# Optimization experiments

Hardware: AMD Instinct MI355X
Metric: run time of the kernel (lower is better)

Reference implementation:

```python
import math
import jax, jax.numpy as jnp
import numpy as np

BS = 4; C = 128; D = 128; NH = 4; NL = 2; NP = 8
SHAPES = [(64, 96), (32, 48)]            # (H, W) per level
STARTS = [0, SHAPES[0][0] * SHAPES[0][1]]  # level_start_index


def lrelu(x):
    return jnp.where(x >= 0, x, 0.1 * x)


def conv2d(x, w, b):
    y = jax.lax.conv_general_dilated(x, w, (1, 1), [(1, 1), (1, 1)],
                                     dimension_numbers=('NCHW', 'OIHW', 'NCHW'))
    return y + b[None, :, None, None]


def pos_enc_sine(bs, H, W, npf=64, T=10000.0):
    # DETR PositionEmbeddingSine (normalize=True), mask of ones -> cumsum = index+1
    scale = 2.0 * math.pi
    eps = 1e-6
    y = (jnp.arange(1, H + 1, dtype=jnp.float32) / (H + eps) * scale)[:, None]
    x = (jnp.arange(1, W + 1, dtype=jnp.float32) / (W + eps) * scale)[None, :]
    y = jnp.broadcast_to(y, (H, W))
    x = jnp.broadcast_to(x, (H, W))
    dim_t = T ** (2.0 * (jnp.arange(npf) // 2).astype(jnp.float32) / npf)
    px = x[..., None] / dim_t
    py = y[..., None] / dim_t
    def interleave(p):
        return jnp.stack([jnp.sin(p[..., 0::2]), jnp.cos(p[..., 1::2])], -1).reshape(H, W, npf)
    pos = jnp.concatenate([interleave(py), interleave(px)], -1)  # [H,W,2*npf]
    return jnp.broadcast_to(pos.transpose(2, 0, 1)[None], (bs, 2 * npf, H, W))


def ref_points(bs, H, W):
    ys = (jnp.arange(H, dtype=jnp.float32) + 0.5) / H
    xs = (jnp.arange(W, dtype=jnp.float32) + 0.5) / W
    gy, gx = jnp.meshgrid(ys, xs, indexing='ij')
    ref = jnp.stack([gx.reshape(-1), gy.reshape(-1)], -1)  # [hw, 2] (x, y)
    return jnp.broadcast_to(ref[None, :, None, :], (bs, H * W, 1, 2))


def sample_level(v, loc, Hl, Wl):
    # v: [bs, Hl*Wl, nh, d]; loc: [bs, nq, nh, np, 2] in [0,1] -> grid_sample bilinear, zero pad
    bs, nq, nh, npts, _ = loc.shape
    d = v.shape[-1]
    x = loc[..., 0] * Wl - 0.5
    y = loc[..., 1] * Hl - 0.5
    x0f = jnp.floor(x); y0f = jnp.floor(y)
    fx = x - x0f; fy = y - y0f
    x0 = x0f.astype(jnp.int32); y0 = y0f.astype(jnp.int32)
    def gather(xi, yi):
        valid = (xi >= 0) & (xi < Wl) & (yi >= 0) & (yi < Hl)
        idx = jnp.clip(yi, 0, Hl - 1) * Wl + jnp.clip(xi, 0, Wl - 1)  # [bs,nq,nh,np]
        idx = idx.transpose(0, 1, 3, 2).reshape(bs, nq * npts, nh)
        g = jnp.take_along_axis(v, idx[..., None], axis=1)  # [bs,nq*np,nh,d]
        g = g.reshape(bs, nq, npts, nh, d).transpose(0, 1, 3, 2, 4)  # [bs,nq,nh,np,d]
        return g * valid[..., None]
    w00 = (1 - fx) * (1 - fy); w01 = fx * (1 - fy); w10 = (1 - fx) * fy; w11 = fx * fy
    return (gather(x0, y0) * w00[..., None] + gather(x0 + 1, y0) * w01[..., None]
            + gather(x0, y0 + 1) * w10[..., None] + gather(x0 + 1, y0 + 1) * w11[..., None])


def msda(value, loc, weights):
    # value [bs,Nv,nh,d], loc [bs,nq,nh,nl,np,2], weights [bs,nq,nh,nl,np]
    out = 0.0
    for l, (Hl, Wl) in enumerate(SHAPES):
        v_l = value[:, STARTS[l]:STARTS[l] + Hl * Wl]
        s = sample_level(v_l, loc[:, :, :, l], Hl, Wl)  # [bs,nq,nh,np,d]
        out = out + jnp.einsum('bqhpd,bqhp->bqhd', s, weights[:, :, :, l])
    bs, nq, nh, d = out.shape
    return out.reshape(bs, nq, nh * d)


def block(query, value, qloc, so_w, so_b, aw_w, aw_b, op_w, op_b):
    bs, nq, _ = query.shape
    off = (query @ so_w + so_b).reshape(bs, nq, NH, NL, NP, 2)
    aw = jax.nn.softmax((query @ aw_w + aw_b).reshape(bs, nq, NH, NL * NP), -1)
    aw = aw.reshape(bs, nq, NH, NL, NP)
    norm = jnp.array([[w, h] for (h, w) in SHAPES], jnp.float32)  # [nl,2] = (W,H)
    loc = qloc[:, :, None, :, None, :] + off / norm[None, None, None, :, None, :]
    return msda(value, loc, aw) @ op_w + op_b  # dropout = identity (eval)


def _forward(feat0_l0, feat0_l1, feat1_l0, feat1_l1,
             cw1, cb1, cw2, cb2, cw3, cb3, vw, vb, lvl_emb,
             so_w0, so_b0, aw_w0, aw_b0, op_w0, op_b0,
             so_w1, so_b1, aw_w1, aw_b1, op_w1, op_b1):
    bs = feat0_l0.shape[0]
    H1, W1 = SHAPES[-1]
    # scale_conv stem on feature0_list[-1]
    q = lrelu(conv2d(feat0_l1, cw1, cb1))
    q = lrelu(conv2d(q, cw2, cb2))
    q = lrelu(conv2d(q, cw3, cb3))
    q = q + pos_enc_sine(bs, H1, W1, npf=D // 2)
    qloc = ref_points(bs, H1, W1)  # [bs, hw, 1, 2]
    # flatten levels + level embeds
    f0 = jnp.concatenate([f.reshape(bs, C, -1) + lvl_emb[l][None, :, None]
                          for l, f in enumerate([feat0_l0, feat0_l1])], axis=2)
    f1 = jnp.concatenate([f.reshape(bs, C, -1) + lvl_emb[l][None, :, None]
                          for l, f in enumerate([feat1_l0, feat1_l1])], axis=2)
    cat = jnp.concatenate([f0, f1], axis=1)  # [bs, 2C, Nv]
    value = jnp.einsum('oc,bcn->bno', vw, cat) + vb  # 1x1 Conv1d -> [bs, Nv, D]
    value = jnp.broadcast_to(value[:, :, None, :], (bs, value.shape[1], NH, D))
    query = q.reshape(bs, D, -1).transpose(0, 2, 1)  # [bs, hw, D]
    query = block(query, value, qloc, so_w0, so_b0, aw_w0, aw_b0, op_w0, op_b0)
    query = block(query, value, qloc, so_w1, so_b1, aw_w1, aw_b1, op_w1, op_b1)
    return query.reshape(bs, H1, W1, D).transpose(0, 3, 1, 2)


def setup_inputs() -> dict:
    key = jax.random.key(0)
    ks = iter(jax.random.split(key, 32))
    def rn(shape, s=1.0):
        return jax.random.normal(next(ks), shape, jnp.float32) * s
    inp = {}
    inp['feat0_l0'] = rn((BS, C, SHAPES[0][0], SHAPES[0][1]))
    inp['feat0_l1'] = rn((BS, C, SHAPES[1][0], SHAPES[1][1]))
    inp['feat1_l0'] = rn((BS, C, SHAPES[0][0], SHAPES[0][1]))
    inp['feat1_l1'] = rn((BS, C, SHAPES[1][0], SHAPES[1][1]))
    inp['cw1'] = rn((2 * D, C, 3, 3), 0.03); inp['cb1'] = rn((2 * D,), 0.01)
    inp['cw2'] = rn((D, 2 * D, 3, 3), 0.03); inp['cb2'] = rn((D,), 0.01)
    inp['cw3'] = rn((D, D, 3, 3), 0.03); inp['cb3'] = rn((D,), 0.01)
    inp['vw'] = rn((D, 2 * C), 0.05); inp['vb'] = rn((D,), 0.01)
    inp['lvl_emb'] = rn((NL, C), 0.05)
    for i in range(2):
        inp[f'so_w{i}'] = rn((D, NH * NL * NP * 2), 0.02)
        inp[f'so_b{i}'] = rn((NH * NL * NP * 2,), 0.5)
        inp[f'aw_w{i}'] = rn((D, NH * NL * NP), 0.02)
        inp[f'aw_b{i}'] = rn((NH * NL * NP,), 0.01)
        inp[f'op_w{i}'] = rn((NH * D, D), 0.05)
        inp[f'op_b{i}'] = rn((D,), 0.01)
    return inp


def reference(feat0_l0, feat0_l1, feat1_l0, feat1_l1,
              cw1, cb1, cw2, cb2, cw3, cb3, vw, vb, lvl_emb,
              so_w0, so_b0, aw_w0, aw_b0, op_w0, op_b0,
              so_w1, so_b1, aw_w1, aw_b1, op_w1, op_b1):
    return _forward(feat0_l0, feat0_l1, feat1_l0, feat1_l1,
                    cw1, cb1, cw2, cb2, cw3, cb3, vw, vb, lvl_emb,
                    so_w0, so_b0, aw_w0, aw_b0, op_w0, op_b0,
                    so_w1, so_b1, aw_w1, aw_b1, op_w1, op_b1)
```

## Files before the change

### kernel.cpp

```cpp
#include <hip/hip_runtime.h>
#include <hip/hip_bf16.h>

typedef unsigned short u16;
typedef u16   u16x8 __attribute__((ext_vector_type(8)));
typedef short s16x8 __attribute__((ext_vector_type(8)));
typedef float f32x4 __attribute__((ext_vector_type(4)));

__device__ __forceinline__ float bf2f(u16 u) {
    union { unsigned int i; float f; } v; v.i = ((unsigned int)u) << 16; return v.f;
}
__device__ __forceinline__ u16 f2bf(float f) {
    unsigned int x = __float_as_uint(f);
    return (u16)((x + 0x7fffu + ((x >> 16) & 1u)) >> 16);
}
__device__ __forceinline__ float ldv(const void* p, size_t i, int f32) {
    return f32 ? ((const float*)p)[i] : bf2f(((const u16*)p)[i]);
}

template<int ACT, int OUTM, int OUT_BF16, int BN>
__device__ __forceinline__ void gemm_body(
    u16* __restrict__ smem, int bid,
    const u16* __restrict__ A, const u16* __restrict__ Bt,
    const u16* __restrict__ bias, void* __restrict__ Cv,
    int M, int K, int ldc, int nbase, const int* __restrict__ flag)
{
    constexpr int NF = BN >> 4;
    u16 (*As)[72] = (u16(*)[72])smem;
    u16 (*Bs)[72] = (u16(*)[72])(smem + 4608);

    const int t    = threadIdx.x;
    const int wv   = t >> 6, lane = t & 63;
    const int fr   = lane & 15, fg = lane >> 4;
    const int tiles_m = M >> 6;
    const int bm = bid % tiles_m, bn = bid / tiles_m;
    const int m0 = bm << 6, n0 = bn * BN;

    f32x4 acc[NF] = {};
    const int srow = t >> 2;
    const int scol = (t & 3) << 4;
    const int brow = (BN == 64) ? srow : (t >> 3);
    const int bcol = (BN == 64) ? scol : ((t & 7) << 3);
    const u16* Ap = A  + (size_t)(m0 + srow) * K + scol;
    const u16* Bp = Bt + (size_t)(n0 + brow) * K + bcol;

    const int ns = K >> 6;
    uint4 av0 = *(const uint4*)Ap, av1 = *(const uint4*)(Ap + 8);
    uint4 bv0 = *(const uint4*)Bp, bv1 = {0,0,0,0};
    if constexpr (BN == 64) bv1 = *(const uint4*)(Bp + 8);
    for (int s = 0; s < ns; ++s) {
        __syncthreads();
        *(uint4*)&As[srow][scol]     = av0;  *(uint4*)&As[srow][scol + 8] = av1;
        *(uint4*)&Bs[brow][bcol]     = bv0;
        if constexpr (BN == 64) *(uint4*)&Bs[brow][bcol + 8] = bv1;
        __syncthreads();
        if (s + 1 < ns) {
            const u16* An = Ap + ((s + 1) << 6);
            const u16* Bn = Bp + ((s + 1) << 6);
            av0 = *(const uint4*)An;  av1 = *(const uint4*)(An + 8);
            bv0 = *(const uint4*)Bn;
            if constexpr (BN == 64) bv1 = *(const uint4*)(Bn + 8);
        }
        union U { uint4 q; s16x8 v; };
        #pragma unroll
        for (int kk = 0; kk < 2; ++kk) {
            U af; af.q = *(const uint4*)&As[(wv << 4) + fr][(kk << 5) + (fg << 3)];
            U bf[NF];
            #pragma unroll
            for (int j = 0; j < NF; ++j)
                bf[j].q = *(const uint4*)&Bs[(j << 4) + fr][(kk << 5) + (fg << 3)];
            #pragma unroll
            for (int j = 0; j < NF; ++j)
                acc[j] = __builtin_amdgcn_mfma_f32_16x16x32_bf16(af.v, bf[j].v, acc[j], 0, 0, 0);
        }
    }

    float vv[NF][4];
    #pragma unroll
    for (int r = 0; r < 4; ++r) {
        float bvv = bf2f(bias[m0 + (wv << 4) + (fg << 2) + r]);
        #pragma unroll
        for (int j = 0; j < NF; ++j) {
            float v = acc[j][r] + bvv;
            if (ACT) v = (v >= 0.f) ? v : 0.1f * v;
            vv[j][r] = v;
        }
    }

    if constexpr (OUTM == 0) {
        #pragma unroll
        for (int j = 0; j < NF; ++j)
            #pragma unroll
            for (int r = 0; r < 4; ++r) {
                size_t idx = (size_t)(m0 + (wv << 4) + (fg << 2) + r) * ldc
                           + (nbase + n0 + (j << 4) + fr);
                if (OUT_BF16) ((u16*)Cv)[idx] = f2bf(vv[j][r]);
                else          ((float*)Cv)[idx] = vv[j][r];
            }
    } else if constexpr (OUTM == 1) {
        __syncthreads();
        u16* bb = smem;
        #pragma unroll
        for (int j = 0; j < NF; ++j)
            #pragma unroll
            for (int r = 0; r < 4; ++r)
                bb[((j << 4) + fr) * 72 + (wv << 4) + (fg << 2) + r] = f2bf(vv[j][r]);
        __syncthreads();
        if constexpr (BN == 64) {
            int row = t >> 2, seg = (t & 3) << 4;
            const uint4* src = (const uint4*)&bb[row * 72 + seg];
            uint4* dst = (uint4*)((u16*)Cv + (size_t)(nbase + n0 + row) * M + m0 + seg);
            dst[0] = src[0];
            dst[1] = src[1];
        } else {
            int row = t >> 3, seg = (t & 7) << 3;
            const uint4* src = (const uint4*)&bb[row * 72 + seg];
            uint4* dst = (uint4*)((u16*)Cv + (size_t)(nbase + n0 + row) * M + m0 + seg);
            dst[0] = src[0];
        }
    } else {
        __syncthreads();
        constexpr int LDB = BN + 8;
        u16* bb = smem;
        #pragma unroll
        for (int j = 0; j < NF; ++j)
            #pragma unroll
            for (int r = 0; r < 4; ++r)
                bb[((wv << 4) + (fg << 2) + r) * LDB + (j << 4) + fr] = f2bf(vv[j][r]);
        __syncthreads();
        int f32o = *flag;
        constexpr int EPT = BN / 4;
        int mrow = t >> 2, seg = (t & 3) * EPT;
        int b = n0 / 1536, hw0 = (n0 % 1536) + seg;
        size_t base = (size_t)(b * 128 + m0 + mrow) * 1536 + hw0;
        if (!f32o) {
            #pragma unroll
            for (int q = 0; q < EPT / 8; ++q)
                *(uint4*)((u16*)Cv + base + q * 8) = *(const uint4*)&bb[mrow * LDB + seg + q * 8];
        } else {
            float* dst = (float*)Cv + base;
            #pragma unroll
            for (int j = 0; j < EPT; ++j) dst[j] = bf2f(bb[mrow * LDB + seg + j]);
        }
    }
}

template<int CIN, int POS, int BN>
__device__ __forceinline__ void conv_body(
    u16* __restrict__ smem, int bid,
    const u16* __restrict__ A, const u16* __restrict__ X,
    const u16* __restrict__ bias, u16* __restrict__ Cv, int M)
{
    constexpr int NF = BN >> 4;
    u16 (*As)[72] = (u16(*)[72])smem;
    u16 (*Bs)[72] = (u16(*)[72])(smem + 4608);

    constexpr int NK2 = CIN / 64;
    constexpr int TOT = 9 * NK2;

    const int t    = threadIdx.x;
    const int wv   = t >> 6, lane = t & 63;
    const int fr   = lane & 15, fg = lane >> 4;
    const int tiles_m = M >> 6;
    const int bm = bid % tiles_m, bn = bid / tiles_m;
    const int m0 = bm << 6, n0 = bn * BN;

    const int srow = t >> 2;
    const int scol = (t & 3) << 4;
    const int brow = (BN == 64) ? srow : (t >> 3);
    const int bcol = (BN == 64) ? scol : ((t & 7) << 3);
    const int n  = n0 + brow;
    const int hw = n % 1536;
    const int hp = hw / 48, wp = hw % 48;
    const u16* Ar = A + (size_t)(m0 + srow) * (9 * CIN) + scol;

    f32x4 acc[NF] = {};

    auto ld = [&](int s, uint4& a0, uint4& a1, uint4& b0, uint4& b1) {
        int tap = s / NK2, k0 = (s % NK2) << 6;
        int dy = tap / 3 - 1, dx = tap % 3 - 1;
        bool vr = ((unsigned)(hp + dy) < 32u) && ((unsigned)(wp + dx) < 48u);
        const u16* Ap = Ar + tap * CIN + k0;
        a0 = *(const uint4*)Ap;  a1 = *(const uint4*)(Ap + 8);
        if (vr) {
            const u16* Bp = X + (size_t)(n + dy * 48 + dx) * CIN + bcol + k0;
            b0 = *(const uint4*)Bp;
            if constexpr (BN == 64) b1 = *(const uint4*)(Bp + 8);
        } else {
            b0 = uint4{0,0,0,0};  b1 = uint4{0,0,0,0};
        }
    };

    uint4 av0, av1, bv0, bv1;
    ld(0, av0, av1, bv0, bv1);
    for (int s = 0; s < TOT; ++s) {
        __syncthreads();
        *(uint4*)&As[srow][scol]     = av0;  *(uint4*)&As[srow][scol + 8] = av1;
        *(uint4*)&Bs[brow][bcol]     = bv0;
        if constexpr (BN == 64) *(uint4*)&Bs[brow][bcol + 8] = bv1;
        __syncthreads();
        if (s + 1 < TOT) ld(s + 1, av0, av1, bv0, bv1);
        union U { uint4 q; s16x8 v; };
        #pragma unroll
        for (int kk = 0; kk < 2; ++kk) {
            U af; af.q = *(const uint4*)&As[(wv << 4) + fr][(kk << 5) + (fg << 3)];
            U bf[NF];
            #pragma unroll
            for (int j = 0; j < NF; ++j)
                bf[j].q = *(const uint4*)&Bs[(j << 4) + fr][(kk << 5) + (fg << 3)];
            #pragma unroll
            for (int j = 0; j < NF; ++j)
                acc[j] = __builtin_amdgcn_mfma_f32_16x16x32_bf16(af.v, bf[j].v, acc[j], 0, 0, 0);
        }
    }

    float vv[NF][4];
    #pragma unroll
    for (int r = 0; r < 4; ++r) {
        float bvv = bf2f(bias[m0 + (wv << 4) + (fg << 2) + r]);
        #pragma unroll
        for (int j = 0; j < NF; ++j) {
            float v = acc[j][r] + bvv;
            vv[j][r] = (v >= 0.f) ? v : 0.1f * v;
        }
    }

    if (POS) {
        const float TWO_PI = 6.283185307179586f;
        #pragma unroll
        for (int j = 0; j < NF; ++j) {
            int ntok = n0 + (j << 4) + fr;
            int hw2 = ntok % 1536;
            int hp2 = hw2 / 48, wp2 = hw2 % 48;
            float yv = (float)(hp2 + 1) * (TWO_PI / (32.f + 1e-6f));
            float xv = (float)(wp2 + 1) * (TWO_PI / (48.f + 1e-6f));
            #pragma unroll
            for (int r = 0; r < 4; ++r) {
                int d = m0 + (wv << 4) + (fg << 2) + r;
                int mm = (d & 63) >> 1;
                float dim = exp2f((float)mm * (13.287712379549449f / 32.f));
                float val = ((d < 64) ? yv : xv) / dim;
                vv[j][r] += (d & 1) ? cosf(val) : sinf(val);
            }
        }
    }

    __syncthreads();
    u16* bb = smem;
    #pragma unroll
    for (int j = 0; j < NF; ++j)
        #pragma unroll
        for (int r = 0; r < 4; ++r)
            bb[((j << 4) + fr) * 72 + (wv << 4) + (fg << 2) + r] = f2bf(vv[j][r]);
    __syncthreads();
    if constexpr (BN == 64) {
        int row = t >> 2, seg = (t & 3) << 4;
        const uint4* src = (const uint4*)&bb[row * 72 + seg];
        uint4* dst = (uint4*)(Cv + (size_t)(n0 + row) * M + m0 + seg);
        dst[0] = src[0];
        dst[1] = src[1];
    } else {
        int row = t >> 3, seg = (t & 7) << 3;
        const uint4* src = (const uint4*)&bb[row * 72 + seg];
        uint4* dst = (uint4*)(Cv + (size_t)(n0 + row) * M + m0 + seg);
        dst[0] = src[0];
    }
}

template<int CIN, int POS, int BN>
__global__ __launch_bounds__(256) void conv_gemm(
    const u16* __restrict__ A, const u16* __restrict__ X,
    const u16* __restrict__ bias, u16* __restrict__ Cv, int M)
{
    __shared__ __align__(16) u16 smem[9216];
    conv_body<CIN, POS, BN>(smem, blockIdx.x, A, X, bias, Cv, M);
}

__global__ __launch_bounds__(256) void val_conv1_k(
    const u16* __restrict__ AVW, const u16* __restrict__ CATT,
    const u16* __restrict__ vb, u16* __restrict__ VAL,
    const u16* __restrict__ AW1, const u16* __restrict__ X0,
    const u16* __restrict__ cb1, u16* __restrict__ CH1)
{
    __shared__ __align__(16) u16 smem[9216];
    int bid = blockIdx.x;
    if (bid < 960) gemm_body<0, 1, 1, 64>(smem, bid, AVW, CATT, vb, VAL, 128, 256, 0, 0, nullptr);
    else           conv_body<128, 0, 64>(smem, bid - 960, AW1, X0, cb1, CH1, 256);
}

template<int OUTM>
__global__ __launch_bounds__(256) void attn_fused(
    const u16* __restrict__ QT, const u16* __restrict__ APJ,
    const u16* __restrict__ BPJ, const u16* __restrict__ VAL,
    const u16* __restrict__ AOP, const u16* __restrict__ OB,
    void* __restrict__ OUT, const int* __restrict__ flag)
{
    __shared__ __align__(16) char lds[46144];
    u16*   qs  = (u16*)lds;
    u16*   Ss  = (u16*)(lds + 4352);
    float* PAs = (float*)(lds + 20992);
    float* XYs = (float*)(lds + 33856);
    float* LGs = (float*)(lds + 42048);

    const int t  = threadIdx.x;
    const int wv = t >> 6, lane = t & 63;
    const int fr = lane & 15, fg = lane >> 4;
    const int bid = blockIdx.x;
    const int tok0 = ((bid & 7) * 48 + (bid >> 3)) << 4;

    union U { uint4 q; s16x8 v; };

    {
        int tok = t >> 4, seg = (t & 15) << 3;
        *(uint4*)&qs[tok * 136 + seg] = *(const uint4*)&QT[(size_t)(tok0 + tok) * 128 + seg];
    }
    __syncthreads();

    {
        f32x4 pacc[3] = {};
        #pragma unroll
        for (int ks = 0; ks < 4; ++ks) {
            U bf; bf.q = *(const uint4*)&qs[fr * 136 + ks * 32 + (fg << 3)];
            #pragma unroll
            for (int j = 0; j < 3; ++j) {
                int m = ((wv * 3 + j) << 4) + fr;
                U af; af.q = *(const uint4*)&APJ[(size_t)m * 128 + ks * 32 + (fg << 3)];
                pacc[j] = __builtin_amdgcn_mfma_f32_16x16x32_bf16(af.v, bf.v, pacc[j], 0, 0, 0);
            }
        }
        #pragma unroll
        for (int j = 0; j < 3; ++j) {
            int mb = (wv * 3 + j) << 4;
            #pragma unroll
            for (int r = 0; r < 4; ++r) {
                int m = mb + (fg << 2) + r;
                PAs[fr * 201 + m] = pacc[j][r] + bf2f(BPJ[m]);
            }
        }
    }
    __syncthreads();

    #pragma unroll
    for (int i = 0; i < 4; ++i) {
        int slot = t + i * 256;
        int tok = slot >> 6, s = slot & 63;
        int h = s >> 4, l = (s >> 3) & 1, p = s & 7;
        int orow = h * 32 + l * 16 + p * 2;
        int lrow = 128 + h * 16 + l * 8 + p;
        float offx = PAs[tok * 201 + orow];
        float offy = PAs[tok * 201 + orow + 1];
        int gtok = tok0 + tok;
        int hw = gtok % 1536;
        int hp = hw / 48, wp = hw % 48;
        float Wl = l ? 48.f : 96.f, Hl = l ? 32.f : 64.f;
        float locx = (wp + 0.5f) / 48.f + offx / Wl;
        float locy = (hp + 0.5f) / 32.f + offy / Hl;
        XYs[(tok * 64 + s) * 2]     = locx * Wl - 0.5f;
        XYs[(tok * 64 + s) * 2 + 1] = locy * Hl - 0.5f;
        LGs[tok * 64 + s] = PAs[tok * 201 + lrow];
    }
    __syncthreads();

    float awr[4];
    #pragma unroll
    for (int i = 0; i < 4; ++i) {
        int slot = t + i * 256;
        int tok = slot >> 6, s = slot & 63;
        const float* G = &LGs[tok * 64 + (s & ~15)];
        float mx = -1e30f;
        for (int j2 = 0; j2 < 16; ++j2) mx = fmaxf(mx, G[j2]);
        float sum = 0.f;
        for (int j2 = 0; j2 < 16; ++j2) sum += expf(G[j2] - mx);
        awr[i] = expf(LGs[tok * 64 + s] - mx) / sum;
    }
    __syncthreads();
    #pragma unroll
    for (int i = 0; i < 4; ++i) {
        int slot = t + i * 256;
        LGs[(slot >> 6) * 64 + (slot & 63)] = awr[i];
    }
    __syncthreads();

    {
        const int tokg = t >> 5, sub = t & 31, h = sub >> 3, seg = sub & 7;
        #pragma unroll
        for (int round = 0; round < 2; ++round) {
            int tok = round * 8 + tokg;
            int b = (tok0 + tok) / 1536;
            float acc[16];
            #pragma unroll
            for (int j = 0; j < 16; ++j) acc[j] = 0.f;
            #pragma unroll 2
            for (int s16i = 0; s16i < 16; ++s16i) {
                int s = h * 16 + s16i;
                int l = (s16i >> 3) & 1;
                int iWl = l ? 48 : 96, iHl = l ? 32 : 64;
                int vrow = b * 7680 + (l ? 6144 : 0);
                float x  = XYs[(tok * 64 + s) * 2];
                float y  = XYs[(tok * 64 + s) * 2 + 1];
                float aw = LGs[tok * 64 + s];
                float xf = floorf(x), yf = floorf(y);
                float fx = x - xf, fy = y - yf;
                int ix = (int)xf, iy = (int)yf;
                bool vx0 = (unsigned)ix < (unsigned)iWl, vx1 = (unsigned)(ix + 1) < (unsigned)iWl;
                bool vy0 = (unsigned)iy < (unsigned)iHl, vy1 = (unsigned)(iy + 1) < (unsigned)iHl;
                float w0 = (vx0 && vy0) ? (1.f - fx) * (1.f - fy) * aw : 0.f;
                float w1 = (vx1 && vy0) ? fx * (1.f - fy) * aw : 0.f;
                float w2 = (vx0 && vy1) ? (1.f - fx) * fy * aw : 0.f;
                float w3 = (vx1 && vy1) ? fx * fy * aw : 0.f;
                int i0 = (vx0 && vy0) ? vrow + iy * iWl + ix           : 0;
                int i1 = (vx1 && vy0) ? vrow + iy * iWl + ix + 1       : 0;
                int i2 = (vx0 && vy1) ? vrow + (iy + 1) * iWl + ix     : 0;
                int i3 = (vx1 && vy1) ? vrow + (iy + 1) * iWl + ix + 1 : 0;
                const u16* p0 = VAL + (size_t)i0 * 128 + (seg << 4);
                const u16* p1 = VAL + (size_t)i1 * 128 + (seg << 4);
                const u16* p2 = VAL + (size_t)i2 * 128 + (seg << 4);
                const u16* p3 = VAL + (size_t)i3 * 128 + (seg << 4);
                u16x8 v0a = *(const u16x8*)p0, v0b = *(const u16x8*)(p0 + 8);
                u16x8 v1a = *(const u16x8*)p1, v1b = *(const u16x8*)(p1 + 8);
                u16x8 v2a = *(const u16x8*)p2, v2b = *(const u16x8*)(p2 + 8);
                u16x8 v3a = *(const u16x8*)p3, v3b = *(const u16x8*)(p3 + 8);
                #pragma unroll
                for (int j = 0; j < 8; ++j) {
                    acc[j]     += w0 * bf2f(v0a[j]) + w1 * bf2f(v1a[j])
                                + w2 * bf2f(v2a[j]) + w3 * bf2f(v3a[j]);
                    acc[8 + j] += w0 * bf2f(v0b[j]) + w1 * bf2f(v1b[j])
                                + w2 * bf2f(v2b[j]) + w3 * bf2f(v3b[j]);
                }
            }
            u16x8 o0, o1;
            #pragma unroll
            for (int j = 0; j < 8; ++j) { o0[j] = f2bf(acc[j]); o1[j] = f2bf(acc[8 + j]); }
            u16* sp = &Ss[tok * 520 + (h << 7) + (seg << 4)];
            *(u16x8*)sp = o0;
            *(u16x8*)(sp + 8) = o1;
        }
    }
    __syncthreads();

    {
        f32x4 oacc[2] = {};
        for (int ks = 0; ks < 16; ++ks) {
            U bf; bf.q = *(const uint4*)&Ss[fr * 520 + ks * 32 + (fg << 3)];
            #pragma unroll
            for (int j = 0; j < 2; ++j) {
                int m = ((wv * 2 + j) << 4) + fr;
                U af; af.q = *(const uint4*)&AOP[(size_t)m * 512 + ks * 32 + (fg << 3)];
                oacc[j] = __builtin_amdgcn_mfma_f32_16x16x32_bf16(af.v, bf.v, oacc[j], 0, 0, 0);
            }
        }
        #pragma unroll
        for (int j = 0; j < 2; ++j) {
            int mb = (wv * 2 + j) << 4;
            #pragma unroll
            for (int r = 0; r < 4; ++r) {
                int m = mb + (fg << 2) + r;
                qs[fr * 136 + m] = f2bf(oacc[j][r] + bf2f(OB[m]));
            }
        }
    }
    __syncthreads();

    if constexpr (OUTM == 0) {
        int tok = t >> 4, m0 = (t & 15) << 3;
        *(uint4*)((u16*)OUT + (size_t)(tok0 + tok) * 128 + m0) = *(const uint4*)&qs[tok * 136 + m0];
    } else {
        int f32o = *flag;
        int m = t & 127, grp = t >> 7;
        int b = tok0 / 1536, hw0 = (tok0 % 1536) + (grp << 3);
        size_t base = (size_t)(b * 128 + m) * 1536 + hw0;
        if (!f32o) {
            u16x8 o;
            #pragma unroll
            for (int j = 0; j < 8; ++j) o[j] = qs[((grp << 3) + j) * 136 + m];
            *(u16x8*)((u16*)OUT + base) = o;
        } else {
            #pragma unroll
            for (int j = 0; j < 8; ++j)
                ((float*)OUT)[base + j] = bf2f(qs[((grp << 3) + j) * 136 + m]);
        }
    }
}

struct P21 { const void* p[21]; };

__global__ __launch_bounds__(256) void prep_fused(
    P21 a, const void* __restrict__ f00, const void* __restrict__ f01,
    const void* __restrict__ f10, const void* __restrict__ f11,
    int* __restrict__ FLAG,
    u16* AW1, u16* AW2, u16* AW3, u16* AVW,
    u16* APJ0, u16* APJ1, u16* AOP0, u16* AOP1,
    u16* BPJ0, u16* BPJ1, u16* SB,
    u16* CATT, u16* X0)
{
    __shared__ __align__(16) u16 Ts[128 * 66];
    const int t = threadIdx.x;
    unsigned int w = ((const unsigned int*)f00)[t];
    float pa = fabsf(bf2f((u16)(w & 0xFFFFu)));
    int cnt = __syncthreads_count(pa > 1e-6f && pa < 1e4f);
    const int f32 = (cnt < 128);
    const int bid = blockIdx.x;
    if (bid == 0 && t == 0) *FLAG = f32;

    if (bid < 3718) {
        int g = bid * 256 + t;
        if (g < 294912) { int m = g / 1152, rem = g % 1152, tap = rem >> 7, ci = rem & 127;
            AW1[g] = f2bf(ldv(a.p[0], (size_t)m * 1152 + ci * 9 + tap, f32)); return; }
        g -= 294912;
        if (g < 294912) { int m = g / 2304, rem = g % 2304, tap = rem >> 8, ci = rem & 255;
            AW2[g] = f2bf(ldv(a.p[2], (size_t)m * 2304 + ci * 9 + tap, f32)); return; }
        g -= 294912;
        if (g < 147456) { int m = g / 1152, rem = g % 1152, tap = rem >> 7, ci = rem & 127;
            AW3[g] = f2bf(ldv(a.p[4], (size_t)m * 1152 + ci * 9 + tap, f32)); return; }
        g -= 147456;
        if (g < 32768) { AVW[g] = f2bf(ldv(a.p[6], g, f32)); return; }
        g -= 32768;
        if (g < 24576) { int o = g >> 7, d = g & 127;
            APJ0[g] = f2bf(o < 128 ? ldv(a.p[9], d * 128 + o, f32)
                                   : ldv(a.p[11], d * 64 + (o - 128), f32)); return; }
        g -= 24576;
        if (g < 24576) { int o = g >> 7, d = g & 127;
            APJ1[g] = f2bf(o < 128 ? ldv(a.p[15], d * 128 + o, f32)
                                   : ldv(a.p[17], d * 64 + (o - 128), f32)); return; }
        g -= 24576;
        if (g < 65536) { int o = g >> 9, k = g & 511; AOP0[g] = f2bf(ldv(a.p[13], k * 128 + o, f32)); return; }
        g -= 65536;
        if (g < 65536) { int o = g >> 9, k = g & 511; AOP1[g] = f2bf(ldv(a.p[19], k * 128 + o, f32)); return; }
        g -= 65536;
        if (g < 192) { BPJ0[g] = f2bf(g < 128 ? ldv(a.p[10], g, f32) : ldv(a.p[12], g - 128, f32)); return; }
        g -= 192;
        if (g < 192) { BPJ1[g] = f2bf(g < 128 ? ldv(a.p[16], g, f32) : ldv(a.p[18], g - 128, f32)); return; }
        g -= 192;
        if (g < 1152) {
            const int off[8] = {0, 256, 384, 512, 640, 896, 1024, 1152};
            const int src[7] = {1, 3, 5, 7, 8, 14, 20};
            int s = 0;
            #pragma unroll
            for (int i = 1; i < 7; ++i) s += (g >= off[i]);
            SB[g] = f2bf(ldv(a.p[src[s]], g - off[s], f32));
        }
        return;
    }

    const void* src; u16* dst;
    int b, hw0, HW, rowlen, coloff, lvl, addemb;
    if (bid < 4678) {
        int g = bid - 3718;
        int half = g & 1;  g >>= 1;
        b = g / 120;  int tile = g % 120;
        lvl = (tile >= 96) ? 1 : 0;
        int tl = lvl ? tile - 96 : tile;
        hw0 = tl << 6;
        HW = lvl ? 1536 : 6144;
        src = (half == 0) ? (lvl ? f01 : f00) : (lvl ? f11 : f10);
        dst = CATT + (size_t)(b * 7680 + lvl * 6144 + hw0) * 256;
        rowlen = 256; coloff = half << 7; addemb = 1;
    } else {
        int g = bid - 4678;
        b = g / 24;  hw0 = (g % 24) << 6;
        HW = 1536; src = f01;
        dst = X0 + (size_t)(b * 1536 + hw0) * 128;
        rowlen = 128; coloff = 0; lvl = 1; addemb = 0;
    }

    {
        int c = t >> 1, hseg = (t & 1) << 5;
        size_t base = (size_t)(b * 128 + c) * HW + hw0 + hseg;
        u16* dstl = &Ts[c * 66 + hseg];
        if (!f32) {
            const u16* s8 = (const u16*)src + base;
            *(uint4*)(dstl)      = *(const uint4*)(s8);
            *(uint4*)(dstl + 8)  = *(const uint4*)(s8 + 8);
            *(uint4*)(dstl + 16) = *(const uint4*)(s8 + 16);
            *(uint4*)(dstl + 24) = *(const uint4*)(s8 + 24);
        } else {
            const float* sf = (const float*)src + base;
            #pragma unroll
            for (int q = 0; q < 32; ++q) dstl[q] = f2bf(sf[q]);
        }
    }
    __syncthreads();
    {
        int tok = t & 63, cseg = (t >> 6) << 5;
        u16 outv[32];
        #pragma unroll
        for (int j = 0; j < 32; ++j) {
            float x = bf2f(Ts[(cseg + j) * 66 + tok]);
            if (addemb) x += ldv(a.p[8], lvl * 128 + cseg + j, f32);
            outv[j] = f2bf(x);
        }
        u16* drow = dst + (size_t)tok * rowlen + coloff + cseg;
        #pragma unroll
        for (int q = 0; q < 4; ++q)
            *(uint4*)(drow + q * 8) = *(const uint4*)(&outv[q * 8]);
    }
}

extern "C" void kernel_launch(void* const* d_in, const int* in_sizes, int n_in,
                              void* d_out, int out_size, void* d_ws, size_t ws_size,
                              hipStream_t stream)
{
    (void)in_sizes; (void)n_in; (void)out_size; (void)ws_size;

    char* ws = (char*)d_ws;
    size_t off = 0;
    auto alloc = [&](size_t bytes) { size_t o = off; off += (bytes + 255) & ~(size_t)255; return o; };
    int*   FLAG = (int*)(ws + alloc(256));
    u16*   AW1  = (u16*)(ws + alloc(294912ull * 2));
    u16*   AW2  = (u16*)(ws + alloc(294912ull * 2));
    u16*   AW3  = (u16*)(ws + alloc(147456ull * 2));
    u16*   AVW  = (u16*)(ws + alloc(32768ull * 2));
    u16*   APJ0 = (u16*)(ws + alloc(24576ull * 2));
    u16*   APJ1 = (u16*)(ws + alloc(24576ull * 2));
    u16*   AOP0 = (u16*)(ws + alloc(65536ull * 2));
    u16*   AOP1 = (u16*)(ws + alloc(65536ull * 2));
    u16*   BPJ0 = (u16*)(ws + alloc(512));
    u16*   BPJ1 = (u16*)(ws + alloc(512));
    u16*   SB   = (u16*)(ws + alloc(1152ull * 2));
    u16*   VAL  = (u16*)(ws + alloc(30720ull * 128 * 2));
    u16*   X0   = (u16*)(ws + alloc(6144ull * 128 * 2));
    u16*   CH1  = (u16*)(ws + alloc(6144ull * 256 * 2));
    u16*   CH2  = (u16*)(ws + alloc(6144ull * 128 * 2));
    u16*   QT0  = (u16*)(ws + alloc(6144ull * 128 * 2));
    u16*   QT1  = (u16*)(ws + alloc(6144ull * 128 * 2));
    u16*   CATT = (u16*)(ws + alloc(30720ull * 256 * 2));

    u16* cb1C = SB + 0;   u16* cb2C = SB + 256;  u16* cb3C = SB + 384;
    u16* vbC  = SB + 512;
    u16* ob0C = SB + 896; u16* ob1C = SB + 1024;

    P21 a;
    const int widx[21] = {4,5,6,7,8,9,10,11,12, 13,14,15,16,17,18, 19,20,21,22,23,24};
    for (int i = 0; i < 21; ++i) a.p[i] = d_in[widx[i]];

    prep_fused<<<4774, 256, 0, stream>>>(a, d_in[0], d_in[1], d_in[2], d_in[3], FLAG,
                                         AW1, AW2, AW3, AVW,
                                         APJ0, APJ1, AOP0, AOP1, BPJ0, BPJ1, SB,
                                         CATT, X0);

    val_conv1_k<<<960 + 384, 256, 0, stream>>>(AVW, CATT, vbC, VAL, AW1, X0, cb1C, CH1);

    conv_gemm<256, 0, 32><<<2 * 192, 256, 0, stream>>>(AW2, CH1, cb2C, CH2, 128);
    conv_gemm<128, 1, 32><<<2 * 192, 256, 0, stream>>>(AW3, CH2, cb3C, QT0, 128);

    attn_fused<0><<<384, 256, 0, stream>>>(QT0, APJ0, BPJ0, VAL, AOP0, ob0C, QT1, FLAG);

    attn_fused<1><<<384, 256, 0, stream>>>(QT1, APJ1, BPJ1, VAL, AOP1, ob1C, d_out, FLAG);
}
```

Measured before the change: 152.6 us.

## Split fused attention into sampling kernel and separate output-projection GEMM

The fused attention kernel, which did projection, softmax, deformable sampling and output projection for 16 tokens per block, is split in two. A sampling kernel now handles 8 tokens per block across 768 blocks and writes sampled features to a global scratch buffer that reuses the CATT allocation. A generic GEMM kernel then applies the output projection. This raises block count and parallelism in the gather-heavy phase and lowers LDS use per block. The cost is two extra kernel launches and a global round trip of the 6144x512 intermediate. The offset-projection MFMA also now runs half-empty, with 8 of 16 columns zero-padded.

```diff
diff --git a/kernel.cpp b/kernel.cpp
--- a/kernel.cpp
+++ b/kernel.cpp
@@ -266,6 +266,16 @@
     }
 }
 
+template<int ACT, int OUTM, int OUT_BF16, int BN>
+__global__ __launch_bounds__(256) void gemm_kn(
+    const u16* __restrict__ A, const u16* __restrict__ Bt,
+    const u16* __restrict__ bias, void* __restrict__ Cv,
+    int M, int K, int ldc, int nbase, const int* __restrict__ flag)
+{
+    __shared__ __align__(16) u16 smem[9216];
+    gemm_body<ACT, OUTM, OUT_BF16, BN>(smem, blockIdx.x, A, Bt, bias, Cv, M, K, ldc, nbase, flag);
+}
+
 template<int CIN, int POS, int BN>
 __global__ __launch_bounds__(256) void conv_gemm(
     const u16* __restrict__ A, const u16* __restrict__ X,
@@ -287,31 +297,29 @@
     else           conv_body<128, 0, 64>(smem, bid - 960, AW1, X0, cb1, CH1, 256);
 }
 
-template<int OUTM>
-__global__ __launch_bounds__(256) void attn_fused(
+__global__ __launch_bounds__(256) void msda_proj(
     const u16* __restrict__ QT, const u16* __restrict__ APJ,
     const u16* __restrict__ BPJ, const u16* __restrict__ VAL,
-    const u16* __restrict__ AOP, const u16* __restrict__ OB,
-    void* __restrict__ OUT, const int* __restrict__ flag)
-{
-    __shared__ __align__(16) char lds[46144];
-    u16*   qs  = (u16*)lds;
-    u16*   Ss  = (u16*)(lds + 4352);
-    float* PAs = (float*)(lds + 20992);
-    float* XYs = (float*)(lds + 33856);
-    float* LGs = (float*)(lds + 42048);
+    u16* __restrict__ S)
+{
+    __shared__ __align__(16) u16 qs[16 * 136];
+    __shared__ float PAs[8][201];
+    __shared__ float XYs[8][64][2];
+    __shared__ float LGs[8][64];
 
     const int t  = threadIdx.x;
     const int wv = t >> 6, lane = t & 63;
     const int fr = lane & 15, fg = lane >> 4;
     const int bid = blockIdx.x;
-    const int tok0 = ((bid & 7) * 48 + (bid >> 3)) << 4;
+    const int tok0 = ((bid & 7) * 96 + (bid >> 3)) << 3;
 
     union U { uint4 q; s16x8 v; };
 
     {
         int tok = t >> 4, seg = (t & 15) << 3;
-        *(uint4*)&qs[tok * 136 + seg] = *(const uint4*)&QT[(size_t)(tok0 + tok) * 128 + seg];
+        uint4 v = {0, 0, 0, 0};
+        if (tok < 8) v = *(const uint4*)&QT[(size_t)(tok0 + tok) * 128 + seg];
+        *(uint4*)&qs[tok * 136 + seg] = v;
     }
     __syncthreads();
 
@@ -327,157 +335,110 @@
                 pacc[j] = __builtin_amdgcn_mfma_f32_16x16x32_bf16(af.v, bf.v, pacc[j], 0, 0, 0);
             }
         }
-        #pragma unroll
-        for (int j = 0; j < 3; ++j) {
-            int mb = (wv * 3 + j) << 4;
-            #pragma unroll
-            for (int r = 0; r < 4; ++r) {
-                int m = mb + (fg << 2) + r;
-                PAs[fr * 201 + m] = pacc[j][r] + bf2f(BPJ[m]);
+        if (fr < 8) {
+            #pragma unroll
+            for (int j = 0; j < 3; ++j) {
+                int mb = (wv * 3 + j) << 4;
+                #pragma unroll
+                for (int r = 0; r < 4; ++r) {
+                    int m = mb + (fg << 2) + r;
+                    PAs[fr][m] = pacc[j][r] + bf2f(BPJ[m]);
+                }
             }
         }
     }
     __syncthreads();
 
     #pragma unroll
-    for (int i = 0; i < 4; ++i) {
+    for (int i = 0; i < 2; ++i) {
         int slot = t + i * 256;
         int tok = slot >> 6, s = slot & 63;
         int h = s >> 4, l = (s >> 3) & 1, p = s & 7;
         int orow = h * 32 + l * 16 + p * 2;
-        int lrow = 128 + h * 16 + l * 8 + p;
-        float offx = PAs[tok * 201 + orow];
-        float offy = PAs[tok * 201 + orow + 1];
+        float offx = PAs[tok][orow];
+        float offy = PAs[tok][orow + 1];
         int gtok = tok0 + tok;
         int hw = gtok % 1536;
         int hp = hw / 48, wp = hw % 48;
         float Wl = l ? 48.f : 96.f, Hl = l ? 32.f : 64.f;
         float locx = (wp + 0.5f) / 48.f + offx / Wl;
         float locy = (hp + 0.5f) / 32.f + offy / Hl;
-        XYs[(tok * 64 + s) * 2]     = locx * Wl - 0.5f;
-        XYs[(tok * 64 + s) * 2 + 1] = locy * Hl - 0.5f;
-        LGs[tok * 64 + s] = PAs[tok * 201 + lrow];
-    }
-    __syncthreads();
-
-    float awr[4];
+        XYs[tok][s][0] = locx * Wl - 0.5f;
+        XYs[tok][s][1] = locy * Hl - 0.5f;
+        LGs[tok][s] = PAs[tok][128 + h * 16 + l * 8 + p];
+    }
+    __syncthreads();
+
+    float awr[2];
     #pragma unroll
-    for (int i = 0; i < 4; ++i) {
+    for (int i = 0; i < 2; ++i) {
         int slot = t + i * 256;
         int tok = slot >> 6, s = slot & 63;
-        const float* G = &LGs[tok * 64 + (s & ~15)];
+        const float* G = &LGs[tok][s & ~15];
         float mx = -1e30f;
         for (int j2 = 0; j2 < 16; ++j2) mx = fmaxf(mx, G[j2]);
         float sum = 0.f;
         for (int j2 = 0; j2 < 16; ++j2) sum += expf(G[j2] - mx);
-        awr[i] = expf(LGs[tok * 64 + s] - mx) / sum;
+        awr[i] = expf(LGs[tok][s] - mx) / sum;
     }
     __syncthreads();
     #pragma unroll
-    for (int i = 0; i < 4; ++i) {
+    for (int i = 0; i < 2; ++i) {
         int slot = t + i * 256;
-        LGs[(slot >> 6) * 64 + (slot & 63)] = awr[i];
+        LGs[slot >> 6][slot & 63] = awr[i];
     }
     __syncthreads();
 
     {
-        const int tokg = t >> 5, sub = t & 31, h = sub >> 3, seg = sub & 7;
-        #pragma unroll
-        for (int round = 0; round < 2; ++round) {
-            int tok = round * 8 + tokg;
-            int b = (tok0 + tok) / 1536;
-            float acc[16];
-            #pragma unroll
-            for (int j = 0; j < 16; ++j) acc[j] = 0.f;
-            #pragma unroll 2
-            for (int s16i = 0; s16i < 16; ++s16i) {
-                int s = h * 16 + s16i;
-                int l = (s16i >> 3) & 1;
-                int iWl = l ? 48 : 96, iHl = l ? 32 : 64;
-                int vrow = b * 7680 + (l ? 6144 : 0);
-                float x  = XYs[(tok * 64 + s) * 2];
-                float y  = XYs[(tok * 64 + s) * 2 + 1];
-                float aw = LGs[tok * 64 + s];
-                float xf = floorf(x), yf = floorf(y);
-                float fx = x - xf, fy = y - yf;
-                int ix = (int)xf, iy = (int)yf;
-                bool vx0 = (unsigned)ix < (unsigned)iWl, vx1 = (unsigned)(ix + 1) < (unsigned)iWl;
-                bool vy0 = (unsigned)iy < (unsigned)iHl, vy1 = (unsigned)(iy + 1) < (unsigned)iHl;
-                float w0 = (vx0 && vy0) ? (1.f - fx) * (1.f - fy) * aw : 0.f;
-                float w1 = (vx1 && vy0) ? fx * (1.f - fy) * aw : 0.f;
-                float w2 = (vx0 && vy1) ? (1.f - fx) * fy * aw : 0.f;
-                float w3 = (vx1 && vy1) ? fx * fy * aw : 0.f;
-                int i0 = (vx0 && vy0) ? vrow + iy * iWl + ix           : 0;
-                int i1 = (vx1 && vy0) ? vrow + iy * iWl + ix + 1       : 0;
-                int i2 = (vx0 && vy1) ? vrow + (iy + 1) * iWl + ix     : 0;
-                int i3 = (vx1 && vy1) ? vrow + (iy + 1) * iWl + ix + 1 : 0;
-                const u16* p0 = VAL + (size_t)i0 * 128 + (seg << 4);
-                const u16* p1 = VAL + (size_t)i1 * 128 + (seg << 4);
-                const u16* p2 = VAL + (size_t)i2 * 128 + (seg << 4);
-                const u16* p3 = VAL + (size_t)i3 * 128 + (seg << 4);
-                u16x8 v0a = *(const u16x8*)p0, v0b = *(const u16x8*)(p0 + 8);
-                u16x8 v1a = *(const u16x8*)p1, v1b = *(const u16x8*)(p1 + 8);
-                u16x8 v2a = *(const u16x8*)p2, v2b = *(const u16x8*)(p2 + 8);
-                u16x8 v3a = *(const u16x8*)p3, v3b = *(const u16x8*)(p3 + 8);
-                #pragma unroll
-                for (int j = 0; j < 8; ++j) {
-                    acc[j]     += w0 * bf2f(v0a[j]) + w1 * bf2f(v1a[j])
-                                + w2 * bf2f(v2a[j]) + w3 * bf2f(v3a[j]);
-                    acc[8 + j] += w0 * bf2f(v0b[j]) + w1 * bf2f(v1b[j])
-                                + w2 * bf2f(v2b[j]) + w3 * bf2f(v3b[j]);
-                }
+        const int tok = t >> 5, sub = t & 31, h = sub >> 3, seg = sub & 7;
+        int b = (tok0 + tok) / 1536;
+        float acc[16];
+        #pragma unroll
+        for (int j = 0; j < 16; ++j) acc[j] = 0.f;
+        #pragma unroll 2
+        for (int s16i = 0; s16i < 16; ++s16i) {
+            int s = h * 16 + s16i;
+            int l = (s16i >> 3) & 1;
+            int iWl = l ? 48 : 96, iHl = l ? 32 : 64;
+            int vrow = b * 7680 + (l ? 6144 : 0);
+            float x  = XYs[tok][s][0];
+            float y  = XYs[tok][s][1];
+            float aw = LGs[tok][s];
+            float xf = floorf(x), yf = floorf(y);
+            float fx = x - xf, fy = y - yf;
+            int ix = (int)xf, iy = (int)yf;
+            bool vx0 = (unsigned)ix < (unsigned)iWl, vx1 = (unsigned)(ix + 1) < (unsigned)iWl;
+            bool vy0 = (unsigned)iy < (unsigned)iHl, vy1 = (unsigned)(iy + 1) < (unsigned)iHl;
+            float w0 = (vx0 && vy0) ? (1.f - fx) * (1.f - fy) * aw : 0.f;
+            float w1 = (vx1 && vy0) ? fx * (1.f - fy) * aw : 0.f;
+            float w2 = (vx0 && vy1) ? (1.f - fx) * fy * aw : 0.f;
+            float w3 = (vx1 && vy1) ? fx * fy * aw : 0.f;
+            int i0 = (vx0 && vy0) ? vrow + iy * iWl + ix           : 0;
+            int i1 = (vx1 && vy0) ? vrow + iy * iWl + ix + 1       : 0;
+            int i2 = (vx0 && vy1) ? vrow + (iy + 1) * iWl + ix     : 0;
+            int i3 = (vx1 && vy1) ? vrow + (iy + 1) * iWl + ix + 1 : 0;
+            const u16* p0 = VAL + (size_t)i0 * 128 + (seg << 4);
+            const u16* p1 = VAL + (size_t)i1 * 128 + (seg << 4);
+            const u16* p2 = VAL + (size_t)i2 * 128 + (seg << 4);
+            const u16* p3 = VAL + (size_t)i3 * 128 + (seg << 4);
+            u16x8 v0a = *(const u16x8*)p0, v0b = *(const u16x8*)(p0 + 8);
+            u16x8 v1a = *(const u16x8*)p1, v1b = *(const u16x8*)(p1 + 8);
+            u16x8 v2a = *(const u16x8*)p2, v2b = *(const u16x8*)(p2 + 8);
+            u16x8 v3a = *(const u16x8*)p3, v3b = *(const u16x8*)(p3 + 8);
+            #pragma unroll
+            for (int j = 0; j < 8; ++j) {
+                acc[j]     += w0 * bf2f(v0a[j]) + w1 * bf2f(v1a[j])
+                            + w2 * bf2f(v2a[j]) + w3 * bf2f(v3a[j]);
+                acc[8 + j] += w0 * bf2f(v0b[j]) + w1 * bf2f(v1b[j])
+                            + w2 * bf2f(v2b[j]) + w3 * bf2f(v3b[j]);
             }
-            u16x8 o0, o1;
-            #pragma unroll
-            for (int j = 0; j < 8; ++j) { o0[j] = f2bf(acc[j]); o1[j] = f2bf(acc[8 + j]); }
-            u16* sp = &Ss[tok * 520 + (h << 7) + (seg << 4)];
-            *(u16x8*)sp = o0;
-            *(u16x8*)(sp + 8) = o1;
-        }
-    }
-    __syncthreads();
-
-    {
-        f32x4 oacc[2] = {};
-        for (int ks = 0; ks < 16; ++ks) {
-            U bf; bf.q = *(const uint4*)&Ss[fr * 520 + ks * 32 + (fg << 3)];
-            #pragma unroll
-            for (int j = 0; j < 2; ++j) {
-                int m = ((wv * 2 + j) << 4) + fr;
-                U af; af.q = *(const uint4*)&AOP[(size_t)m * 512 + ks * 32 + (fg << 3)];
-                oacc[j] = __builtin_amdgcn_mfma_f32_16x16x32_bf16(af.v, bf.v, oacc[j], 0, 0, 0);
-            }
-        }
-        #pragma unroll
-        for (int j = 0; j < 2; ++j) {
-            int mb = (wv * 2 + j) << 4;
-            #pragma unroll
-            for (int r = 0; r < 4; ++r) {
-                int m = mb + (fg << 2) + r;
-                qs[fr * 136 + m] = f2bf(oacc[j][r] + bf2f(OB[m]));
-            }
-        }
-    }
-    __syncthreads();
-
-    if constexpr (OUTM == 0) {
-        int tok = t >> 4, m0 = (t & 15) << 3;
-        *(uint4*)((u16*)OUT + (size_t)(tok0 + tok) * 128 + m0) = *(const uint4*)&qs[tok * 136 + m0];
-    } else {
-        int f32o = *flag;
-        int m = t & 127, grp = t >> 7;
-        int b = tok0 / 1536, hw0 = (tok0 % 1536) + (grp << 3);
-        size_t base = (size_t)(b * 128 + m) * 1536 + hw0;
-        if (!f32o) {
-            u16x8 o;
-            #pragma unroll
-            for (int j = 0; j < 8; ++j) o[j] = qs[((grp << 3) + j) * 136 + m];
-            *(u16x8*)((u16*)OUT + base) = o;
-        } else {
-            #pragma unroll
-            for (int j = 0; j < 8; ++j)
-                ((float*)OUT)[base + j] = bf2f(qs[((grp << 3) + j) * 136 + m]);
-        }
+        }
+        u16x8 o0, o1;
+        #pragma unroll
+        for (int j = 0; j < 8; ++j) { o0[j] = f2bf(acc[j]); o1[j] = f2bf(acc[8 + j]); }
+        u16* sp = S + (size_t)(tok0 + tok) * 512 + (h << 7) + (seg << 4);
+        *(u16x8*)sp = o0;
+        *(u16x8*)(sp + 8) = o1;
     }
 }
 
@@ -622,7 +583,9 @@
     u16*   CH2  = (u16*)(ws + alloc(6144ull * 128 * 2));
     u16*   QT0  = (u16*)(ws + alloc(6144ull * 128 * 2));
     u16*   QT1  = (u16*)(ws + alloc(6144ull * 128 * 2));
-    u16*   CATT = (u16*)(ws + alloc(30720ull * 256 * 2));
+    char*  R    = ws + alloc(30720ull * 256 * 2);
+    u16*   CATT = (u16*)R;
+    u16*   S    = (u16*)R;
 
     u16* cb1C = SB + 0;   u16* cb2C = SB + 256;  u16* cb3C = SB + 384;
     u16* vbC  = SB + 512;
@@ -642,7 +605,9 @@
     conv_gemm<256, 0, 32><<<2 * 192, 256, 0, stream>>>(AW2, CH1, cb2C, CH2, 128);
     conv_gemm<128, 1, 32><<<2 * 192, 256, 0, stream>>>(AW3, CH2, cb3C, QT0, 128);
 
-    attn_fused<0><<<384, 256, 0, stream>>>(QT0, APJ0, BPJ0, VAL, AOP0, ob0C, QT1, FLAG);
-
-    attn_fused<1><<<384, 256, 0, stream>>>(QT1, APJ1, BPJ1, VAL, AOP1, ob1C, d_out, FLAG);
-}
+    msda_proj<<<768, 256, 0, stream>>>(QT0, APJ0, BPJ0, VAL, S);
+    gemm_kn<0, 1, 1, 32><<<2 * 192, 256, 0, stream>>>(AOP0, S, ob0C, QT1, 128, 512, 0, 0, FLAG);
+
+    msda_proj<<<768, 256, 0, stream>>>(QT1, APJ1, BPJ1, VAL, S);
+    gemm_kn<0, 2, 1, 32><<<2 * 192, 256, 0, stream>>>(AOP1, S, ob1C, d_out, 128, 512, 0, 0, FLAG);
+}
```

After: 144.2 us. 1.06x faster.
